# Optimization experiments

Hardware: AMD Instinct MI355X
Metric: run time of the kernel (lower is better)

Reference implementation:

```python
import jax, jax.numpy as jnp
import numpy as np

B, C, L = 8, 256, 2048


def setup_inputs() -> dict:
    key = jax.random.key(0)
    ks = jax.random.split(key, 7)
    s = 0.05
    return {
        "x": jax.random.normal(ks[0], (B, C, L), dtype=jnp.float32),
        "Wq": jax.random.normal(ks[1], (C, C), dtype=jnp.float32) * s,
        "bq": jax.random.normal(ks[2], (C,), dtype=jnp.float32) * s,
        "Wk": jax.random.normal(ks[3], (C, C), dtype=jnp.float32) * s,
        "bk": jax.random.normal(ks[4], (C,), dtype=jnp.float32) * s,
        "Wv": jax.random.normal(ks[5], (C, C), dtype=jnp.float32) * s,
        "bv": jax.random.normal(ks[6], (C,), dtype=jnp.float32) * s,
    }


def reference(x, Wq, bq, Wk, bk, Wv, bv):
    # Conv1d with kernel_size=1 == per-position linear over channels.
    # x: [B, C, L]
    scale = x.shape[1] ** (-0.5)
    q = jnp.einsum('oc,bcl->bol', Wq, x) + bq[None, :, None]  # [B,C,L]
    k = jnp.einsum('oc,bcl->bol', Wk, x) + bk[None, :, None]
    v = jnp.einsum('oc,bcl->bol', Wv, x) + bv[None, :, None]
    scores = jnp.einsum('bcl,bcm->blm', q, k) * scale          # [B,L,L]
    attn = jax.nn.softmax(scores, axis=-1)
    context = jnp.einsum('blm,bcm->bcl', attn, v)              # [B,C,L]
    return context + x
```

## Files before the change

### kernel.cpp

```cpp
#include <hip/hip_runtime.h>

#define NB 8
#define NC 256
#define NL 2048
#define SCALE 0.0625f

typedef __attribute__((ext_vector_type(8))) __bf16 bf16x8;
typedef __attribute__((ext_vector_type(4))) float f32x4;
typedef __attribute__((ext_vector_type(4))) unsigned int u32x4;
typedef __attribute__((ext_vector_type(2))) unsigned int u32x2;
typedef __attribute__((ext_vector_type(4))) unsigned short u16x4;
typedef __attribute__((ext_vector_type(8))) unsigned short u16x8;

static __device__ __forceinline__ unsigned short f2b(float f) {
    unsigned int u = __builtin_bit_cast(unsigned int, f);
    u += 0x7fffu + ((u >> 16) & 1u);
    return (unsigned short)(u >> 16);
}

__global__ void wconv_kernel(const float* __restrict__ Wq,
                             const float* __restrict__ Wk,
                             const float* __restrict__ Wv,
                             unsigned short* __restrict__ Wbf)
{
    const int base = (blockIdx.x * 256 + threadIdx.x) * 4;
    const int mat  = base >> 16;
    const int off  = base & 65535;
    const float* W = (mat == 0) ? Wq : (mat == 1) ? Wk : Wv;
    float4 w = *(const float4*)&W[off];
    u16x4 p = {f2b(w.x), f2b(w.y), f2b(w.z), f2b(w.w)};
    *(u16x4*)&Wbf[base] = p;
}

__global__ __launch_bounds__(256, 2) void xprep_kernel(
    const float* __restrict__ x, unsigned short* __restrict__ xT)
{
    const int b  = blockIdx.z;
    const int c0 = blockIdx.y * 64;
    const int l0 = blockIdx.x * 64;
    const int t  = threadIdx.x;

    __shared__ unsigned short Tr[64][68];

    #pragma unroll
    for (int p = 0; p < 4; ++p) {
        const int c  = p * 16 + (t >> 4);
        const int lg = t & 15;
        float4 xv = *(const float4*)&x[((size_t)(b * NC + c0 + c)) * NL + l0 + lg * 4];
        u16x4 pk = {f2b(xv.x), f2b(xv.y), f2b(xv.z), f2b(xv.w)};
        *(u16x4*)&Tr[c][lg * 4] = pk;
    }
    __syncthreads();
    #pragma unroll
    for (int j = 0; j < 2; ++j) {
        const int chunk = t + 256 * j;
        const int l  = chunk >> 3;
        const int ck = chunk & 7;
        u16x8 o;
        #pragma unroll
        for (int i = 0; i < 8; ++i) o[i] = Tr[ck * 8 + i][l];
        *(u16x8*)&xT[((size_t)(b * NL + l0 + l)) * NC + c0 + ck * 8] = o;
    }
}

__global__ __launch_bounds__(256, 2) void qkv_mfma(
    const unsigned short* __restrict__ xT,
    const unsigned short* __restrict__ Wbf,
    const float* __restrict__ bq, const float* __restrict__ bk,
    const float* __restrict__ bv,
    unsigned short* __restrict__ qT, unsigned short* __restrict__ kT,
    unsigned short* __restrict__ vo)
{
    const int raw = blockIdx.x;
    const int b   = raw & 7;
    const int rem = raw >> 3;
    const int mat = rem >> 5;
    const int lt0 = (rem & 31) * 64;
    const int t    = threadIdx.x;
    const int w    = t >> 6;
    const int lane = t & 63;
    const int ln15 = lane & 15;
    const int quad = lane >> 4;

    __shared__ __align__(16) unsigned short XT[64 * 256];
    __shared__ __align__(16) unsigned short WC[256 * 64];

    const unsigned short* Wm = Wbf + mat * 65536;
    const float* bias = (mat == 0) ? bq : (mat == 1) ? bk : bv;

    float bvals[4][4];
    #pragma unroll
    for (int ot = 0; ot < 4; ++ot)
        #pragma unroll
        for (int r = 0; r < 4; ++r)
            bvals[ot][r] = bias[w * 64 + ot * 16 + quad * 4 + r];

    #pragma unroll
    for (int s = 0; s < 8; ++s) {
        const int il = w * 8 + s;
        const int n  = il * 2 + (lane >> 5);
        const int p  = lane & 31;
        const int g  = p ^ (n & 15);
        const unsigned short* gp = &xT[((size_t)(b * NL + lt0 + n)) * NC + g * 8];
        __builtin_amdgcn_global_load_lds(
            (const __attribute__((address_space(1))) unsigned int*)gp,
            (__attribute__((address_space(3))) unsigned int*)&XT[il * 512],
            16, 0, 0);
    }

    f32x4 acc[4][4];
    #pragma unroll
    for (int i = 0; i < 4; ++i)
        #pragma unroll
        for (int j = 0; j < 4; ++j) acc[i][j] = f32x4{0.f, 0.f, 0.f, 0.f};

    for (int k0 = 0; k0 < 4; ++k0) {
        if (k0) __syncthreads();
        #pragma unroll
        for (int s = 0; s < 8; ++s) {
            const int il = w * 8 + s;
            const int o  = il * 8 + (lane >> 3);
            const int p  = lane & 7;
            const int g  = p ^ (o & 7);
            const unsigned short* gp = &Wm[(size_t)o * NC + k0 * 64 + g * 8];
            __builtin_amdgcn_global_load_lds(
                (const __attribute__((address_space(1))) unsigned int*)gp,
                (__attribute__((address_space(3))) unsigned int*)&WC[il * 512],
                16, 0, 0);
        }
        __syncthreads();

        #pragma unroll
        for (int ks = 0; ks < 2; ++ks) {
            bf16x8 xf[4];
            #pragma unroll
            for (int lt = 0; lt < 4; ++lt) {
                const int l  = lt * 16 + ln15;
                const int kc = k0 * 8 + ks * 4 + quad;
                const int pp = kc ^ (l & 15);
                xf[lt] = __builtin_bit_cast(bf16x8, *(const u32x4*)&XT[l * 256 + pp * 8]);
            }
            #pragma unroll
            for (int ot = 0; ot < 4; ++ot) {
                const int o  = w * 64 + ot * 16 + ln15;
                const int pp = (ks * 4 + quad) ^ (o & 7);
                bf16x8 wf = __builtin_bit_cast(bf16x8, *(const u32x4*)&WC[o * 64 + pp * 8]);
                #pragma unroll
                for (int lt = 0; lt < 4; ++lt)
                    acc[ot][lt] = __builtin_amdgcn_mfma_f32_16x16x32_bf16(
                                      wf, xf[lt], acc[ot][lt], 0, 0, 0);
            }
        }
    }

    if (mat < 2) {
        unsigned short* out = (mat == 0) ? qT : kT;
        #pragma unroll
        for (int ot = 0; ot < 4; ++ot) {
            const int o_base = w * 64 + ot * 16 + quad * 4;
            #pragma unroll
            for (int lt = 0; lt < 4; ++lt) {
                const int l = lt0 + lt * 16 + ln15;
                u16x4 pk;
                #pragma unroll
                for (int r = 0; r < 4; ++r)
                    pk[r] = f2b(acc[ot][lt][r] + bvals[ot][r]);
                *(u16x4*)&out[((size_t)(b * NL + l)) * NC + o_base] = pk;
            }
        }
    } else {
        #pragma unroll
        for (int ot = 0; ot < 4; ++ot)
            #pragma unroll
            for (int lt = 0; lt < 4; ++lt) {
                const int l = lt0 + lt * 16 + ln15;
                #pragma unroll
                for (int r = 0; r < 4; ++r) {
                    const int o = w * 64 + ot * 16 + quad * 4 + r;
                    vo[((size_t)(b * NC + o)) * NL + l] = f2b(acc[ot][lt][r] + bvals[ot][r]);
                }
            }
    }
}

__global__ __launch_bounds__(1024, 4) void attn_kernel(
    const unsigned short* __restrict__ qT,
    const unsigned short* __restrict__ kT,
    const unsigned short* __restrict__ v,
    const float* __restrict__ x,
    float* __restrict__ out)
{
    const int raw  = blockIdx.x;
    const int b    = raw & 7;
    const int l0   = (raw >> 3) * 64;
    const int t    = threadIdx.x;
    const int w    = t >> 6;
    const int lane = t & 63;
    const int ln15 = lane & 15;
    const int quad = lane >> 4;
    const int qg   = w & 3;
    const int kg   = w >> 2;

    __shared__ __align__(16) char smem[139264];
    unsigned short* Kb0 = (unsigned short*)smem;
    unsigned short* Kb1 = (unsigned short*)(smem + 32768);
    unsigned short* Vb0 = (unsigned short*)(smem + 65536);
    unsigned short* Vb1 = (unsigned short*)(smem + 98304);
    char* Plds = smem + 131072;
    float (*buf)[68] = (float(*)[68])smem;

    bf16x8 qf[8];
    {
        const size_t qrow = ((size_t)b * NL + l0 + qg * 16 + ln15) * NC;
        #pragma unroll
        for (int kt = 0; kt < 8; ++kt)
            qf[kt] = __builtin_bit_cast(bf16x8,
                        *(const u32x4*)&qT[qrow + kt * 32 + quad * 8]);
    }

    f32x4 ctx[4];
    #pragma unroll
    for (int i = 0; i < 4; ++i) ctx[i] = f32x4{0.f, 0.f, 0.f, 0.f};
    f32x4 dacc = f32x4{0.f, 0.f, 0.f, 0.f};

    const u16x8 ones_u = {0x3F80, 0x3F80, 0x3F80, 0x3F80,
                          0x3F80, 0x3F80, 0x3F80, 0x3F80};
    const bf16x8 onesf = __builtin_bit_cast(bf16x8, ones_u);

    auto stage = [&](int mt, unsigned short* Kd, unsigned short* Vd) {
        const int m0 = mt * 64;
        #pragma unroll
        for (int s = 0; s < 2; ++s) {
            const int il = w * 2 + s;
            const int n  = il * 2 + (lane >> 5);
            const int g  = (lane & 31) ^ (n & 15);
            const unsigned short* gp = &kT[((size_t)b * NL + m0 + n) * NC + g * 8];
            __builtin_amdgcn_global_load_lds(
                (const __attribute__((address_space(1))) unsigned int*)gp,
                (__attribute__((address_space(3))) unsigned int*)&Kd[il * 512],
                16, 0, 0);
        }
        #pragma unroll
        for (int s = 0; s < 2; ++s) {
            const int il = w * 2 + s;
            const int c  = il * 8 + (lane >> 3);
            const int g  = (lane & 7) ^ (c & 7);
            const unsigned short* gp = &v[((size_t)(b * NC + c)) * NL + m0 + g * 8];
            __builtin_amdgcn_global_load_lds(
                (const __attribute__((address_space(1))) unsigned int*)gp,
                (__attribute__((address_space(3))) unsigned int*)&Vd[il * 512],
                16, 0, 0);
        }
    };

    stage(0, Kb0, Vb0);
    __syncthreads();

    const int q    = qg * 16 + ln15;
    const int pwof = q * 128 + (((kg * 32) + quad * 8) ^ ((q & 7) << 4));
    int prof[2];
    #pragma unroll
    for (int jw = 0; jw < 2; ++jw)
        prof[jw] = q * 128 + ((jw * 64 + quad * 16) ^ ((q & 7) << 4));

    for (int mt = 0; mt < 32; ++mt) {
        if (mt < 31) {
            if (mt & 1) stage(mt + 1, Kb0, Vb0);
            else        stage(mt + 1, Kb1, Vb1);
        }
        const unsigned short* Kd = (mt & 1) ? Kb1 : Kb0;
        const unsigned short* Vd = (mt & 1) ? Vb1 : Vb0;

        f32x4 sacc = f32x4{0.f, 0.f, 0.f, 0.f};
        {
            const int n = kg * 16 + ln15;
            #pragma unroll
            for (int kt = 0; kt < 8; ++kt) {
                const int p = (kt * 4 + quad) ^ (n & 15);
                bf16x8 kf = __builtin_bit_cast(bf16x8,
                              *(const u32x4*)&Kd[n * 256 + p * 8]);
                sacc = __builtin_amdgcn_mfma_f32_16x16x32_bf16(
                           kf, qf[kt], sacc, 0, 0, 0);
            }
        }

        {
            float e0 = __expf(sacc[0] * SCALE);
            float e1 = __expf(sacc[1] * SCALE);
            float e2 = __expf(sacc[2] * SCALE);
            float e3 = __expf(sacc[3] * SCALE);
            unsigned int d0 = (unsigned int)f2b(e0) | ((unsigned int)f2b(e1) << 16);
            unsigned int d1 = (unsigned int)f2b(e2) | ((unsigned int)f2b(e3) << 16);
            *(u32x2*)(Plds + pwof) = u32x2{d0, d1};
        }

        asm volatile("s_waitcnt lgkmcnt(0)" ::: "memory");
        __builtin_amdgcn_s_barrier();
        __builtin_amdgcn_sched_barrier(0);

        bf16x8 pa[2];
        #pragma unroll
        for (int jw = 0; jw < 2; ++jw)
            pa[jw] = __builtin_bit_cast(bf16x8, *(const u32x4*)(Plds + prof[jw]));

        dacc = __builtin_amdgcn_mfma_f32_16x16x32_bf16(pa[0], onesf, dacc, 0, 0, 0);
        dacc = __builtin_amdgcn_mfma_f32_16x16x32_bf16(pa[1], onesf, dacc, 0, 0, 0);

        #pragma unroll
        for (int ct = 0; ct < 4; ++ct) {
            const int c = kg * 64 + ct * 16 + ln15;
            #pragma unroll
            for (int jw = 0; jw < 2; ++jw) {
                const int p = (jw * 4 + quad) ^ (c & 7);
                bf16x8 vb = __builtin_bit_cast(bf16x8,
                              *(const u32x4*)&Vd[c * 64 + p * 8]);
                ctx[ct] = __builtin_amdgcn_mfma_f32_16x16x32_bf16(
                              pa[jw], vb, ctx[ct], 0, 0, 0);
            }
        }

        __syncthreads();
    }

    {
        float rinv[4];
        #pragma unroll
        for (int r = 0; r < 4; ++r) rinv[r] = 1.0f / dacc[r];
        #pragma unroll
        for (int ct = 0; ct < 4; ++ct) {
            const int c = kg * 64 + ct * 16 + ln15;
            #pragma unroll
            for (int r = 0; r < 4; ++r)
                buf[c][qg * 16 + quad * 4 + r] = ctx[ct][r] * rinv[r];
        }
    }
    __syncthreads();

    #pragma unroll
    for (int p = 0; p < 4; ++p) {
        const int f  = t + 1024 * p;
        const int c  = f >> 4;
        const int lg = (f & 15) * 4;
        const size_t idx = ((size_t)(b * NC + c)) * NL + l0 + lg;
        float4 xv = *(const float4*)&x[idx];
        float4 cv = *(const float4*)&buf[c][lg];
        float4 o = make_float4(cv.x + xv.x, cv.y + xv.y, cv.z + xv.z, cv.w + xv.w);
        *(float4*)&out[idx] = o;
    }
}

extern "C" void kernel_launch(void* const* d_in, const int* in_sizes, int n_in,
                              void* d_out, int out_size, void* d_ws, size_t ws_size,
                              hipStream_t stream) {
    const float* x  = (const float*)d_in[0];
    const float* Wq = (const float*)d_in[1];
    const float* bq = (const float*)d_in[2];
    const float* Wk = (const float*)d_in[3];
    const float* bk = (const float*)d_in[4];
    const float* Wv = (const float*)d_in[5];
    const float* bv = (const float*)d_in[6];
    float* out = (float*)d_out;

    const size_t plane = (size_t)NB * NC * NL;
    unsigned short* qT  = (unsigned short*)d_ws;
    unsigned short* kT  = qT + plane;
    unsigned short* v   = kT + plane;
    unsigned short* xT  = v + plane;
    unsigned short* Wbf = xT + plane;

    wconv_kernel<<<192, 256, 0, stream>>>(Wq, Wk, Wv, Wbf);

    dim3 gx(NL / 64, NC / 64, NB);
    xprep_kernel<<<gx, 256, 0, stream>>>(x, xT);

    qkv_mfma<<<768, 256, 0, stream>>>(xT, Wbf, bq, bk, bv, qT, kT, v);

    attn_kernel<<<256, 1024, 0, stream>>>(qT, kT, v, x, out);
}
```

Before: 154.1 us.

## Warp-specialize attention into QK, PV and loader waves with 32x32 MFMA

```diff
diff --git a/kernel.cpp b/kernel.cpp
--- a/kernel.cpp
+++ b/kernel.cpp
@@ -7,6 +7,7 @@
 
 typedef __attribute__((ext_vector_type(8))) __bf16 bf16x8;
 typedef __attribute__((ext_vector_type(4))) float f32x4;
+typedef __attribute__((ext_vector_type(16))) float f32x16;
 typedef __attribute__((ext_vector_type(4))) unsigned int u32x4;
 typedef __attribute__((ext_vector_type(2))) unsigned int u32x2;
 typedef __attribute__((ext_vector_type(4))) unsigned short u16x4;
@@ -196,53 +197,58 @@
     const int t    = threadIdx.x;
     const int w    = t >> 6;
     const int lane = t & 63;
-    const int ln15 = lane & 15;
-    const int quad = lane >> 4;
-    const int qg   = w & 3;
-    const int kg   = w >> 2;
-
-    __shared__ __align__(16) char smem[139264];
+    const int c31  = lane & 31;
+    const int h    = lane >> 5;
+
+    __shared__ __align__(16) char smem[147968];
     unsigned short* Kb0 = (unsigned short*)smem;
     unsigned short* Kb1 = (unsigned short*)(smem + 32768);
     unsigned short* Vb0 = (unsigned short*)(smem + 65536);
     unsigned short* Vb1 = (unsigned short*)(smem + 98304);
-    char* Plds = smem + 131072;
+    char* P0 = smem + 131072;
+    char* P1 = smem + 139264;
+    float* denomP = (float*)(smem + 147456);
     float (*buf)[68] = (float(*)[68])smem;
 
-    bf16x8 qf[8];
-    {
-        const size_t qrow = ((size_t)b * NL + l0 + qg * 16 + ln15) * NC;
-        #pragma unroll
-        for (int kt = 0; kt < 8; ++kt)
-            qf[kt] = __builtin_bit_cast(bf16x8,
-                        *(const u32x4*)&qT[qrow + kt * 32 + quad * 8]);
-    }
-
-    f32x4 ctx[4];
-    #pragma unroll
-    for (int i = 0; i < 4; ++i) ctx[i] = f32x4{0.f, 0.f, 0.f, 0.f};
-    f32x4 dacc = f32x4{0.f, 0.f, 0.f, 0.f};
-
-    const u16x8 ones_u = {0x3F80, 0x3F80, 0x3F80, 0x3F80,
-                          0x3F80, 0x3F80, 0x3F80, 0x3F80};
-    const bf16x8 onesf = __builtin_bit_cast(bf16x8, ones_u);
-
-    auto stage = [&](int mt, unsigned short* Kd, unsigned short* Vd) {
+    const bool isQK = (w < 4);
+    const bool isPV = (w >= 4) && (w < 12);
+    const int qkqh = w >> 1;
+    const int kh   = w & 1;
+    const int pvqh = (w - 4) >> 2;
+    const int cbase = ((w - 4) & 3) * 64;
+
+    bf16x8 qf[16];
+    if (isQK) {
+        const size_t qrow = ((size_t)b * NL + l0 + qkqh * 32 + c31) * NC;
+        #pragma unroll
+        for (int s = 0; s < 16; ++s)
+            qf[s] = __builtin_bit_cast(bf16x8,
+                        *(const u32x4*)&qT[qrow + s * 16 + h * 8]);
+    }
+
+    f32x16 ctxA = {};
+    f32x16 ctxB = {};
+    float dacc = 0.f;
+
+    auto stageK = [&](int mt, unsigned short* Kd) {
         const int m0 = mt * 64;
         #pragma unroll
-        for (int s = 0; s < 2; ++s) {
-            const int il = w * 2 + s;
-            const int n  = il * 2 + (lane >> 5);
-            const int g  = (lane & 31) ^ (n & 15);
+        for (int s = 0; s < 8; ++s) {
+            const int il = (w - 12) * 8 + s;
+            const int n  = il * 2 + h;
+            const int g  = c31 ^ (n & 15);
             const unsigned short* gp = &kT[((size_t)b * NL + m0 + n) * NC + g * 8];
             __builtin_amdgcn_global_load_lds(
                 (const __attribute__((address_space(1))) unsigned int*)gp,
                 (__attribute__((address_space(3))) unsigned int*)&Kd[il * 512],
                 16, 0, 0);
         }
-        #pragma unroll
-        for (int s = 0; s < 2; ++s) {
-            const int il = w * 2 + s;
+    };
+    auto stageV = [&](int mt, unsigned short* Vd) {
+        const int m0 = mt * 64;
+        #pragma unroll
+        for (int s = 0; s < 8; ++s) {
+            const int il = (w - 12) * 8 + s;
             const int c  = il * 8 + (lane >> 3);
             const int g  = (lane & 7) ^ (c & 7);
             const unsigned short* gp = &v[((size_t)(b * NC + c)) * NL + m0 + g * 8];
@@ -253,85 +259,86 @@
         }
     };
 
-    stage(0, Kb0, Vb0);
+    if (w >= 12) stageK(0, Kb0);
     __syncthreads();
 
-    const int q    = qg * 16 + ln15;
-    const int pwof = q * 128 + (((kg * 32) + quad * 8) ^ ((q & 7) << 4));
-    int prof[2];
-    #pragma unroll
-    for (int jw = 0; jw < 2; ++jw)
-        prof[jw] = q * 128 + ((jw * 64 + quad * 16) ^ ((q & 7) << 4));
-
-    for (int mt = 0; mt < 32; ++mt) {
-        if (mt < 31) {
-            if (mt & 1) stage(mt + 1, Kb0, Vb0);
-            else        stage(mt + 1, Kb1, Vb1);
-        }
-        const unsigned short* Kd = (mt & 1) ? Kb1 : Kb0;
-        const unsigned short* Vd = (mt & 1) ? Vb1 : Vb0;
-
-        f32x4 sacc = f32x4{0.f, 0.f, 0.f, 0.f};
-        {
-            const int n = kg * 16 + ln15;
-            #pragma unroll
-            for (int kt = 0; kt < 8; ++kt) {
-                const int p = (kt * 4 + quad) ^ (n & 15);
-                bf16x8 kf = __builtin_bit_cast(bf16x8,
-                              *(const u32x4*)&Kd[n * 256 + p * 8]);
-                sacc = __builtin_amdgcn_mfma_f32_16x16x32_bf16(
-                           kf, qf[kt], sacc, 0, 0, 0);
-            }
-        }
-
-        {
-            float e0 = __expf(sacc[0] * SCALE);
-            float e1 = __expf(sacc[1] * SCALE);
-            float e2 = __expf(sacc[2] * SCALE);
-            float e3 = __expf(sacc[3] * SCALE);
-            unsigned int d0 = (unsigned int)f2b(e0) | ((unsigned int)f2b(e1) << 16);
-            unsigned int d1 = (unsigned int)f2b(e2) | ((unsigned int)f2b(e3) << 16);
-            *(u32x2*)(Plds + pwof) = u32x2{d0, d1};
-        }
-
-        asm volatile("s_waitcnt lgkmcnt(0)" ::: "memory");
-        __builtin_amdgcn_s_barrier();
-        __builtin_amdgcn_sched_barrier(0);
-
-        bf16x8 pa[2];
-        #pragma unroll
-        for (int jw = 0; jw < 2; ++jw)
-            pa[jw] = __builtin_bit_cast(bf16x8, *(const u32x4*)(Plds + prof[jw]));
-
-        dacc = __builtin_amdgcn_mfma_f32_16x16x32_bf16(pa[0], onesf, dacc, 0, 0, 0);
-        dacc = __builtin_amdgcn_mfma_f32_16x16x32_bf16(pa[1], onesf, dacc, 0, 0, 0);
-
-        #pragma unroll
-        for (int ct = 0; ct < 4; ++ct) {
-            const int c = kg * 64 + ct * 16 + ln15;
-            #pragma unroll
-            for (int jw = 0; jw < 2; ++jw) {
-                const int p = (jw * 4 + quad) ^ (c & 7);
-                bf16x8 vb = __builtin_bit_cast(bf16x8,
-                              *(const u32x4*)&Vd[c * 64 + p * 8]);
-                ctx[ct] = __builtin_amdgcn_mfma_f32_16x16x32_bf16(
-                              pa[jw], vb, ctx[ct], 0, 0, 0);
+    const int qq = qkqh * 32 + c31;
+    const int pq = pvqh * 32 + c31;
+
+    for (int r = 0; r <= 32; ++r) {
+        if (w >= 12) {
+            if (r < 31) stageK(r + 1, ((r + 1) & 1) ? Kb1 : Kb0);
+            if (r < 32) stageV(r, (r & 1) ? Vb1 : Vb0);
+        } else if (isQK) {
+            if (r < 32) {
+                const unsigned short* Kd = (r & 1) ? Kb1 : Kb0;
+                char* Pw = (r & 1) ? P1 : P0;
+                const int n = kh * 32 + c31;
+                f32x16 sacc = {};
+                #pragma unroll
+                for (int s = 0; s < 16; ++s) {
+                    const int g = (s * 2 + h) ^ (n & 15);
+                    bf16x8 kf = __builtin_bit_cast(bf16x8,
+                                  *(const u32x4*)&Kd[n * 256 + g * 8]);
+                    sacc = __builtin_amdgcn_mfma_f32_32x32x16_bf16(
+                               kf, qf[s], sacc, 0, 0, 0);
+                }
+                float rs = 0.f;
+                #pragma unroll
+                for (int kr = 0; kr < 4; ++kr) {
+                    float e0 = __expf(sacc[kr * 4 + 0] * SCALE);
+                    float e1 = __expf(sacc[kr * 4 + 1] * SCALE);
+                    float e2 = __expf(sacc[kr * 4 + 2] * SCALE);
+                    float e3 = __expf(sacc[kr * 4 + 3] * SCALE);
+                    rs += (e0 + e1) + (e2 + e3);
+                    unsigned int d0 = (unsigned int)f2b(e0) | ((unsigned int)f2b(e1) << 16);
+                    unsigned int d1 = (unsigned int)f2b(e2) | ((unsigned int)f2b(e3) << 16);
+                    const int s16 = (kh * 4 + kr) ^ (qq & 7);
+                    *(u32x2*)(Pw + qq * 128 + s16 * 16 + 8 * h) = u32x2{d0, d1};
+                }
+                rs += __shfl_xor(rs, 32, 64);
+                dacc += rs;
+            }
+        } else {
+            if (r > 0) {
+                const char* Pr = ((r - 1) & 1) ? P1 : P0;
+                const unsigned short* Vd = ((r - 1) & 1) ? Vb1 : Vb0;
+                #pragma unroll
+                for (int ks = 0; ks < 4; ++ks) {
+                    const int sp = (ks * 2 + h) ^ (pq & 7);
+                    bf16x8 pa = __builtin_bit_cast(bf16x8,
+                                  *(const u32x4*)(Pr + pq * 128 + sp * 16));
+                    const int cA = cbase + c31;
+                    const int gA = (ks * 2 + h) ^ (cA & 7);
+                    bf16x8 vbA = __builtin_bit_cast(bf16x8,
+                                   *(const u32x4*)&Vd[cA * 64 + gA * 8]);
+                    ctxA = __builtin_amdgcn_mfma_f32_32x32x16_bf16(
+                               pa, vbA, ctxA, 0, 0, 0);
+                    const int cB = cbase + 32 + c31;
+                    const int gB = (ks * 2 + h) ^ (cB & 7);
+                    bf16x8 vbB = __builtin_bit_cast(bf16x8,
+                                   *(const u32x4*)&Vd[cB * 64 + gB * 8]);
+                    ctxB = __builtin_amdgcn_mfma_f32_32x32x16_bf16(
+                               pa, vbB, ctxB, 0, 0, 0);
+                }
             }
         }
 
         __syncthreads();
     }
 
-    {
-        float rinv[4];
-        #pragma unroll
-        for (int r = 0; r < 4; ++r) rinv[r] = 1.0f / dacc[r];
-        #pragma unroll
-        for (int ct = 0; ct < 4; ++ct) {
-            const int c = kg * 64 + ct * 16 + ln15;
-            #pragma unroll
-            for (int r = 0; r < 4; ++r)
-                buf[c][qg * 16 + quad * 4 + r] = ctx[ct][r] * rinv[r];
+    if (isQK && lane < 32)
+        denomP[kh * 64 + qkqh * 32 + c31] = dacc;
+    __syncthreads();
+
+    if (isPV) {
+        #pragma unroll
+        for (int reg = 0; reg < 16; ++reg) {
+            const int ql = (reg & 3) + 8 * (reg >> 2) + 4 * h;
+            const int qg = pvqh * 32 + ql;
+            const float rinv = 1.0f / (denomP[qg] + denomP[64 + qg]);
+            buf[cbase + c31][qg]      = ctxA[reg] * rinv;
+            buf[cbase + 32 + c31][qg] = ctxB[reg] * rinv;
         }
     }
     __syncthreads();
```

Measured after the change: 220.0 us. 1.43x slower.
